# Performance work log

Hardware: AMD Instinct MI355X
Metric: run time of the kernel (lower is better)

Reference implementation:

```python
import jax, jax.numpy as jnp
import numpy as np

N_BINS = 50
FEATURE_ID = 0
EPS = 1e-7  # keras backend epsilon used by binary_crossentropy clipping


def setup_inputs() -> dict:
    key = jax.random.key(0)
    k1, k2 = jax.random.split(key)
    inputs = jax.random.normal(k1, (8_000_000, 4), dtype=jnp.float32)
    targets = jax.random.randint(k2, (8_000_000,), 0, 2, dtype=jnp.int32)
    return {"inputs": inputs, "targets": targets}


def _cut_forward(inputs, targets):
    # x: selected feature column, y: binary labels
    x = inputs[:, FEATURE_ID]
    y = targets
    N = x.shape[0]
    n_f = jnp.float32(N)

    x_min = jnp.min(x)
    x_max = jnp.max(x)
    E = N_BINS + 1
    edges = jnp.linspace(x_min, x_max, E)

    # Sort events once; prefix-sum of signal labels gives exact class counts
    # below/above any threshold (equivalent to the per-bin compare+count loop,
    # including the original's inclusive [lower, upper] double-counting of edges).
    order = jnp.argsort(x)
    xs = x[order]
    ys = (y[order] == 1).astype(jnp.float32)
    cs = jnp.concatenate([jnp.zeros((1,), jnp.float32), jnp.cumsum(ys)])  # [N+1]
    Ns = cs[-1]
    Nb = n_f - Ns

    r = jnp.searchsorted(xs, edges, side='right')  # count(x <= e)
    l = jnp.searchsorted(xs, edges, side='left')   # count(x <  e)
    ns_le = cs[r]
    ns_lt = cs[l]
    nb_le = r.astype(jnp.float32) - ns_le
    nb_lt = l.astype(jnp.float32) - ns_lt

    # hist[i] = count(lower[i] <= v <= upper[i]) per class
    hist0 = nb_le[1:] - nb_lt[:-1]  # background, [N_BINS]
    hist1 = ns_le[1:] - ns_lt[:-1]  # signal

    # candidate bin edges: sign-flip boundaries of hist0>hist1 with non-empty bins
    gt0 = hist0 > hist1
    cand0 = jnp.logical_xor(gt0[:-1], gt0[1:]) & (hist0[:-1] > 0)
    gt1 = hist1 > hist0
    cand1 = jnp.logical_xor(gt1[:-1], gt1[1:]) & (hist1[:-1] > 0)
    mask = jnp.zeros((E,), bool).at[1:N_BINS].set(cand0 | cand1)
    cnt = jnp.sum(mask)
    # original appends x_max when exactly one candidate survives
    mask = mask.at[-1].set(mask[-1] | (cnt == 1))

    # clipped BCE on hard 0/1 predictions reduces to a weighted error count:
    # correct sample -> -log(1-eps), wrong sample -> -log(eps)
    a = -jnp.log1p(jnp.float32(-EPS))
    b = -jnp.log(jnp.float32(EPS))

    def bce(correct):
        return ((n_f - correct) * b + correct * a) / n_f

    # per-edge losses for single-threshold cases
    c0 = ns_le + (Nb - nb_le)          # case 0: pred = (x <= c)
    c1 = (Ns - ns_lt) + nb_lt          # case 1: pred = (x >= c)
    # per-pair losses (i = lower cut, j = upper cut)
    c2 = (ns_le[None, :] - ns_lt[:, None]) + Nb - (nb_le[None, :] - nb_lt[:, None])
    c3 = ns_le[:, None] + (Ns - ns_lt[None, :]) + (nb_le[None, :] - nb_lt[:, None])

    L = jnp.stack([
        jnp.broadcast_to(bce(c0)[:, None], (E, E)),
        jnp.broadcast_to(bce(c1)[:, None], (E, E)),
        bce(c2),
        bce(c3),
    ])  # [4, E, E]
    per_pair_min = jnp.min(L, axis=0)
    per_pair_case = jnp.argmin(L, axis=0)

    idx = jnp.arange(E)
    valid = mask[:, None] & mask[None, :] & (idx[:, None] < idx[None, :])
    flat = jnp.argmin(jnp.where(valid, per_pair_min, jnp.inf))
    i = flat // E
    j = flat % E
    lower = edges[i]
    upper = edges[j]
    case = per_pair_case[i, j]

    pred0 = x <= lower
    pred1 = x >= lower
    pred2 = pred1 & (x <= upper)
    pred3 = pred0 | (x >= upper)
    y_pred = jnp.where(case == 0, pred0,
             jnp.where(case == 1, pred1,
             jnp.where(case == 2, pred2, pred3)))
    return y_pred


def reference(inputs, targets):
    return _cut_forward(inputs, targets).astype(jnp.int32)
```

## Files before the change

kernel.cpp:

```cpp
#include <hip/hip_runtime.h>
#include <math.h>
#include <stdint.h>

#define N_BINS 50
#define EDGE_N 51
#define HIST_N 52
#define NBLK 2048
#define NTHR 256

typedef unsigned int u32;
typedef unsigned short u16;
typedef unsigned char u8;
typedef float f32x4 __attribute__((ext_vector_type(4)));


#define KEEP16(v) asm volatile("" :: "v"(v))

__device__ __forceinline__ float edge_at(int e, float xmin, float xmax) {
  if (e >= N_BINS) return xmax;
  float step = __fdiv_rn((float)e, (float)N_BINS);
  float omst = __fsub_rn(1.0f, step);
  return __fadd_rn(__fmul_rn(xmin, omst), __fmul_rn(xmax, step));
}

__device__ __forceinline__ float bce_f(int c, float n_f, float aC, float bC) {
  float cf = (float)c;
  float t = __fadd_rn(__fmul_rn(__fsub_rn(n_f, cf), bC), __fmul_rn(cf, aC));
  return __fdiv_rn(t, n_f);
}

__device__ __forceinline__ void get_ab(float& aC, float& bC) {
  const double epsd = (double)1e-7f;
  aC = (float)(-log1p(-epsd));
  bC = (float)(-log(epsd));
}

__device__ __forceinline__ void global_minmax(const float* __restrict__ bmin,
                                              const float* __restrict__ bmax,
                                              float* s_red, float* s_mm) {
  const int tid = threadIdx.x;
  float m = INFINITY, M = -INFINITY;
  for (int i = tid; i < NBLK; i += NTHR) { m = fminf(m, bmin[i]); M = fmaxf(M, bmax[i]); }
  for (int off = 32; off; off >>= 1) {
    m = fminf(m, __shfl_down(m, off));
    M = fmaxf(M, __shfl_down(M, off));
  }
  int wid = tid >> 6;
  if ((tid & 63) == 0) { s_red[wid] = m; s_red[4 + wid] = M; }
  __syncthreads();
  if (tid == 0) {
    float mm = s_red[0], MM = s_red[4];
    for (int w = 1; w < NTHR / 64; ++w) { mm = fminf(mm, s_red[w]); MM = fmaxf(MM, s_red[4 + w]); }
    s_mm[0] = mm;
    s_mm[1] = MM;
  }
  __syncthreads();
}

template <int COMPACT>
__global__ void k_minmax(const f32x4* __restrict__ in4, int n,
                         float* __restrict__ bmin, float* __restrict__ bmax,
                         int* __restrict__ histU, int* __restrict__ histE,
                         float* __restrict__ xc) {
  const int tid = threadIdx.x, bid = blockIdx.x;
  const int gid = bid * NTHR + tid;
  const int T = NBLK * NTHR;
  if (bid == 0) {
    for (int i = tid; i < 2 * HIST_N; i += NTHR) histU[i] = 0;
    for (int i = tid; i < 2 * EDGE_N; i += NTHR) histE[i] = 0;
  }
  float vmin = INFINITY, vmax = -INFINITY;
#pragma unroll 4
  for (int i = gid; i < n; i += T) {
    f32x4 r = in4[i];
    KEEP16(r);
    float x = r.x;
    vmin = fminf(vmin, x);
    vmax = fmaxf(vmax, x);
    if (COMPACT) xc[i] = x;
  }
  for (int off = 32; off; off >>= 1) {
    vmin = fminf(vmin, __shfl_down(vmin, off));
    vmax = fmaxf(vmax, __shfl_down(vmax, off));
  }
  __shared__ float s_red[8];
  int wid = tid >> 6;
  if ((tid & 63) == 0) { s_red[wid] = vmin; s_red[4 + wid] = vmax; }
  __syncthreads();
  if (tid == 0) {
    float m = s_red[0], M = s_red[4];
    for (int w = 1; w < NTHR / 64; ++w) { m = fminf(m, s_red[w]); M = fmaxf(M, s_red[4 + w]); }
    bmin[bid] = m;
    bmax[bid] = M;
  }
}

template <int COMPACT>
__global__ void k_hist(const f32x4* __restrict__ in4, const float* __restrict__ xc,
                       const int* __restrict__ tgt, int n,
                       const float* __restrict__ bmin, const float* __restrict__ bmax,
                       int* __restrict__ histU, int* __restrict__ histE,
                       u8* __restrict__ codes) {
  __shared__ u16 ph[HIST_N][NTHR];
  __shared__ float s_edges[EDGE_N];
  __shared__ int shE[2 * EDGE_N];
  __shared__ float s_red[8];
  __shared__ float s_mm[2];
  const int tid = threadIdx.x, bid = blockIdx.x;
  global_minmax(bmin, bmax, s_red, s_mm);
  u32* ph32w = (u32*)&ph[0][0];
  for (int i = tid; i < HIST_N * (NTHR / 2); i += NTHR) ph32w[i] = 0;
  for (int i = tid; i < 2 * EDGE_N; i += NTHR) shE[i] = 0;
  const float xmin = s_mm[0], xmax = s_mm[1];
  if (tid < EDGE_N) s_edges[tid] = edge_at(tid, xmin, xmax);
  __syncthreads();
  const float delta = __fdiv_rn(__fsub_rn(xmax, xmin), (float)N_BINS);
  const float inv_delta = (delta > 0.0f) ? (1.0f / delta) : 0.0f;
  const int gid = bid * NTHR + tid;
  const int T = NBLK * NTHR;
  const int nv = n >> 2;
  const int base = nv << 2;
  const f32x4* __restrict__ xc4 = (const f32x4*)xc;
  const int4* __restrict__ tgt4 = (const int4*)tgt;
  uchar4* __restrict__ codes4 = (uchar4*)codes;
  for (int iv = gid; iv < nv; iv += T) {
    float xs[4];
    if (COMPACT) {
      f32x4 v = xc4[iv];
      xs[0] = v.x; xs[1] = v.y; xs[2] = v.z; xs[3] = v.w;
    } else {
      f32x4 a = in4[4 * iv + 0], b = in4[4 * iv + 1], c = in4[4 * iv + 2], d = in4[4 * iv + 3];
      xs[0] = a.x; xs[1] = b.x; xs[2] = c.x; xs[3] = d.x;
    }
    int4 tv = tgt4[iv];
    int ts[4] = {tv.x, tv.y, tv.z, tv.w};
    u8 cd[4];
#pragma unroll
    for (int k = 0; k < 4; ++k) {
      float x = xs[k];
      int cls = (ts[k] == 1) ? 0 : 1;
      int g = (int)((x - xmin) * inv_delta);
      g = max(0, min(g, EDGE_N));
      while (g < EDGE_N && s_edges[g] < x) ++g;
      while (g > 0 && s_edges[g - 1] >= x) --g;
      int eq = (g < EDGE_N && s_edges[g] == x) ? 1 : 0;
      ph[g][tid] = (u16)(ph[g][tid] + (1u << (cls * 8)));
      if (eq) atomicAdd(&shE[cls * EDGE_N + g], 1);
      cd[k] = (u8)(g | (eq << 6));
    }
    if (COMPACT) codes4[iv] = make_uchar4(cd[0], cd[1], cd[2], cd[3]);
  }
  if (bid == 0 && tid < (n - base)) {
    int i = base + tid;
    float x = COMPACT ? xc[i] : in4[i].x;
    int cls = (tgt[i] == 1) ? 0 : 1;
    int g = (int)((x - xmin) * inv_delta);
    g = max(0, min(g, EDGE_N));
    while (g < EDGE_N && s_edges[g] < x) ++g;
    while (g > 0 && s_edges[g - 1] >= x) --g;
    int eq = (g < EDGE_N && s_edges[g] == x) ? 1 : 0;
    ph[g][tid] = (u16)(ph[g][tid] + (1u << (cls * 8)));
    if (eq) atomicAdd(&shE[cls * EDGE_N + g], 1);
    if (COMPACT) codes[i] = (u8)(g | (eq << 6));
  }
  __syncthreads();
  if (tid < HIST_N) {
    const u32* ph32r = (const u32*)&ph[0][0];
    u32 c0 = 0, c1 = 0;
    for (int k2 = 0; k2 < NTHR / 2; ++k2) {
      int idx = (k2 + tid) & (NTHR / 2 - 1);
      u32 w = ph32r[tid * (NTHR / 2) + idx];
      c0 += (w & 0xFFu) + ((w >> 16) & 0xFFu);
      c1 += ((w >> 8) & 0xFFu) + ((w >> 24) & 0xFFu);
    }
    if (c0) atomicAdd(&histU[tid], (int)c0);
    if (c1) atomicAdd(&histU[HIST_N + tid], (int)c1);
  }
  for (int kk = tid; kk < 2 * EDGE_N; kk += NTHR) {
    int v = shE[kk];
    if (v) atomicAdd(&histE[kk], v);
  }
}

template <int COMPACT>
__global__ void k_decide_pred(const f32x4* __restrict__ in4, const u8* __restrict__ codes,
                              int n, const float* __restrict__ bmin,
                              const float* __restrict__ bmax,
                              const int* __restrict__ histU, const int* __restrict__ histE,
                              int* __restrict__ out) {
  __shared__ float s_red[8];
  __shared__ float s_mm[2];
  __shared__ int s_ns_le[EDGE_N], s_ns_lt[EDGE_N], s_nb_le[EDGE_N], s_nb_lt[EDGE_N];
  __shared__ int s_h0[N_BINS], s_h1[N_BINS];
  __shared__ unsigned char s_g0[N_BINS], s_g1[N_BINS];
  __shared__ unsigned char s_mask[EDGE_N];
  __shared__ float s_rv[NTHR];
  __shared__ int s_ri[NTHR];
  __shared__ int s_cut[3];
  const int tid = threadIdx.x, bid = blockIdx.x;

  global_minmax(bmin, bmax, s_red, s_mm);

  if (tid < 128) {
    const int lane = tid & 63;
    const int w = tid >> 6;
    int v = (lane < EDGE_N) ? histU[w * HIST_N + lane] : 0;
#pragma unroll
    for (int d = 1; d < 64; d <<= 1) {
      int t = __shfl_up(v, d);
      if (lane >= d) v += t;
    }
    if (lane < EDGE_N) {
      int e = histE[w * EDGE_N + lane];
      if (w == 0) { s_ns_le[lane] = v; s_ns_lt[lane] = v - e; }
      else        { s_nb_le[lane] = v; s_nb_lt[lane] = v - e; }
    }
  }
  if (tid < EDGE_N) s_mask[tid] = 0;
  __syncthreads();
  if (tid < N_BINS) {
    int h0 = s_nb_le[tid + 1] - s_nb_lt[tid];
    int h1 = s_ns_le[tid + 1] - s_ns_lt[tid];
    s_h0[tid] = h0;
    s_h1[tid] = h1;
    s_g0[tid] = h0 > h1;
    s_g1[tid] = h1 > h0;
  }
  __syncthreads();
  if (tid < 64) {
    bool cand = false;
    if (tid + 1 < N_BINS) {
      bool c0 = (s_g0[tid] != s_g0[tid + 1]) && (s_h0[tid] > 0);
      bool c1 = (s_g1[tid] != s_g1[tid + 1]) && (s_h1[tid] > 0);
      cand = c0 || c1;
      if (cand) s_mask[tid + 1] = 1;
    }
    unsigned long long bal = __ballot(cand);
    if (tid == 0 && __popcll(bal) == 1) s_mask[N_BINS] = 1;
  }
  __syncthreads();
  const int Ns = s_ns_le[EDGE_N - 1];
  const int Nb = n - Ns;
  float aC, bC;
  get_ab(aC, bC);
  const float n_f = (float)n;
  float best = INFINITY;
  int bestIdx = 0x7fffffff;
  for (int p = tid; p < EDGE_N * EDGE_N; p += NTHR) {
    int i = p / EDGE_N, j = p - i * EDGE_N;
    float v = INFINITY;
    if (s_mask[i] && s_mask[j] && i < j) {
      int c0 = s_ns_le[i] + (Nb - s_nb_le[i]);
      int c1 = Ns - s_ns_lt[i] + s_nb_lt[i];
      int c2 = s_ns_le[j] - s_ns_lt[i] + Nb - (s_nb_le[j] - s_nb_lt[i]);
      int c3 = s_ns_le[i] + Ns - s_ns_lt[j] + s_nb_le[j] - s_nb_lt[i];
      float L0 = bce_f(c0, n_f, aC, bC);
      float L1 = bce_f(c1, n_f, aC, bC);
      float L2 = bce_f(c2, n_f, aC, bC);
      float L3 = bce_f(c3, n_f, aC, bC);
      v = L0;
      if (L1 < v) v = L1;
      if (L2 < v) v = L2;
      if (L3 < v) v = L3;
    }
    if (v < best || (v == best && p < bestIdx)) { best = v; bestIdx = p; }
  }
  s_rv[tid] = best;
  s_ri[tid] = bestIdx;
  __syncthreads();
  for (int s = NTHR / 2; s > 0; s >>= 1) {
    if (tid < s) {
      float ov = s_rv[tid + s];
      int oi = s_ri[tid + s];
      if (ov < s_rv[tid] || (ov == s_rv[tid] && oi < s_ri[tid])) {
        s_rv[tid] = ov;
        s_ri[tid] = oi;
      }
    }
    __syncthreads();
  }
  if (tid == 0) {
    int p = s_ri[0];
    int i = p / EDGE_N, j = p - i * EDGE_N;
    int c0 = s_ns_le[i] + (Nb - s_nb_le[i]);
    int c1 = Ns - s_ns_lt[i] + s_nb_lt[i];
    int c2 = s_ns_le[j] - s_ns_lt[i] + Nb - (s_nb_le[j] - s_nb_lt[i]);
    int c3 = s_ns_le[i] + Ns - s_ns_lt[j] + s_nb_le[j] - s_nb_lt[i];
    float L0 = bce_f(c0, n_f, aC, bC);
    float L1 = bce_f(c1, n_f, aC, bC);
    float L2 = bce_f(c2, n_f, aC, bC);
    float L3 = bce_f(c3, n_f, aC, bC);
    int cs = 0;
    float m = L0;
    if (L1 < m) { m = L1; cs = 1; }
    if (L2 < m) { m = L2; cs = 2; }
    if (L3 < m) { m = L3; cs = 3; }
    s_cut[0] = cs;
    s_cut[1] = i;
    s_cut[2] = j;
  }
  __syncthreads();

  const int cs = s_cut[0], ci = s_cut[1], cj = s_cut[2];
  const int gid = bid * NTHR + tid;
  const int T = NBLK * NTHR;
  if (COMPACT) {
    const uchar4* __restrict__ c4 = (const uchar4*)codes;
    int4* __restrict__ out4 = (int4*)out;
    const int nv = n >> 2;
    for (int iv = gid; iv < nv; iv += T) {
      uchar4 c = c4[iv];
      u8 bys[4] = {c.x, c.y, c.z, c.w};
      int r[4];
#pragma unroll
      for (int b = 0; b < 4; ++b) {
        int u = (int)(bys[b] & 63u);
        int v = u + (int)(bys[b] >> 6);
        bool p0 = (u <= ci), p1 = (ci < v);
        bool p = (cs == 0) ? p0 : (cs == 1) ? p1 : (cs == 2) ? (p1 && (u <= cj)) : (p0 || (cj < v));
        r[b] = p ? 1 : 0;
      }
      out4[iv] = make_int4(r[0], r[1], r[2], r[3]);
    }
    const int cbase = (n >> 2) << 2;
    if (bid == 0 && tid < (n - cbase)) {
      int i = cbase + tid;
      u32 by = codes[i];
      int u = (int)(by & 63u);
      int v = u + (int)(by >> 6);
      bool p0 = (u <= ci), p1 = (ci < v);
      bool p = (cs == 0) ? p0 : (cs == 1) ? p1 : (cs == 2) ? (p1 && (u <= cj)) : (p0 || (cj < v));
      out[i] = p ? 1 : 0;
    }
  } else {
    const float xmin = s_mm[0], xmax = s_mm[1];
    const float lower = edge_at(ci, xmin, xmax);
    const float upper = edge_at(cj, xmin, xmax);
    for (int i = gid; i < n; i += T) {
      f32x4 r = in4[i];
      float x = r.x;
      bool p;
      if (cs == 0) p = (x <= lower);
      else if (cs == 1) p = (x >= lower);
      else if (cs == 2) p = (x >= lower) && (x <= upper);
      else p = (x <= lower) || (x >= upper);
      out[i] = p ? 1 : 0;
    }
  }
}

extern "C" void kernel_launch(void* const* d_in, const int* in_sizes, int n_in,
                              void* d_out, int out_size, void* d_ws, size_t ws_size,
                              hipStream_t stream) {
  const f32x4* in4 = (const f32x4*)d_in[0];
  const int* tgt = (const int*)d_in[1];
  int n = in_sizes[1];
  int* out = (int*)d_out;
  char* ws = (char*)d_ws;
  float* bmin = (float*)ws;
  float* bmax = (float*)(ws + 8192);
  int* histU = (int*)(ws + 16448);
  int* histE = histU + 2 * HIST_N;
  u8* codes = (u8*)(ws + 32768);
  size_t xcOff = ((size_t)32768 + (size_t)n + 15) & ~(size_t)15;
  float* xc = (float*)(ws + xcOff);
  const bool compact = ws_size >= xcOff + (size_t)n * 4u;

  if (compact) {
    k_minmax<1><<<NBLK, NTHR, 0, stream>>>(in4, n, bmin, bmax, histU, histE, xc);
    k_hist<1><<<NBLK, NTHR, 0, stream>>>(in4, xc, tgt, n, bmin, bmax, histU, histE, codes);
    k_decide_pred<1><<<NBLK, NTHR, 0, stream>>>(in4, codes, n, bmin, bmax, histU, histE, out);
  } else {
    k_minmax<0><<<NBLK, NTHR, 0, stream>>>(in4, n, bmin, bmax, histU, histE, nullptr);
    k_hist<0><<<NBLK, NTHR, 0, stream>>>(in4, nullptr, tgt, n, bmin, bmax, histU, histE, nullptr);
    k_decide_pred<0><<<NBLK, NTHR, 0, stream>>>(in4, nullptr, n, bmin, bmax, histU, histE, out);
  }
}
```

Baseline: 108.6 us.

## Fuse three kernels into one cooperative persistent kernel with grid barriers

Merges the min/max, histogram and decide/predict kernels into a single cooperative launch. Inter-phase dependencies are handled by custom grid barriers built on atomic counters. Global min/max now goes through order-preserving encoded atomicMin/Max instead of a per-block array, and histogram atomics are spread over 16 replicas to reduce contention. A small init kernel is added and the grid is capped by an occupancy query, which trades launch gaps and extra global round trips for spin-wait barrier cost and fewer blocks.

```diff
diff --git a/kernel.cpp b/kernel.cpp
--- a/kernel.cpp
+++ b/kernel.cpp
@@ -5,8 +5,9 @@
 #define N_BINS 50
 #define EDGE_N 51
 #define HIST_N 52
-#define NBLK 2048
 #define NTHR 256
+#define MAXBLK 1280
+#define NREP 16
 
 typedef unsigned int u32;
 typedef unsigned short u16;
@@ -15,6 +16,15 @@
 
 
 #define KEEP16(v) asm volatile("" :: "v"(v))
+
+__device__ __forceinline__ u32 f32_enc(float f) {
+  u32 u = __float_as_uint(f);
+  return (u & 0x80000000u) ? ~u : (u | 0x80000000u);
+}
+__device__ __forceinline__ float f32_dec(u32 k) {
+  u32 u = (k & 0x80000000u) ? (k & 0x7fffffffu) : ~k;
+  return __uint_as_float(u);
+}
 
 __device__ __forceinline__ float edge_at(int e, float xmin, float xmax) {
   if (e >= N_BINS) return xmax;
@@ -35,40 +45,58 @@
   bC = (float)(-log(epsd));
 }
 
-__device__ __forceinline__ void global_minmax(const float* __restrict__ bmin,
-                                              const float* __restrict__ bmax,
-                                              float* s_red, float* s_mm) {
-  const int tid = threadIdx.x;
-  float m = INFINITY, M = -INFINITY;
-  for (int i = tid; i < NBLK; i += NTHR) { m = fminf(m, bmin[i]); M = fmaxf(M, bmax[i]); }
-  for (int off = 32; off; off >>= 1) {
-    m = fminf(m, __shfl_down(m, off));
-    M = fmaxf(M, __shfl_down(M, off));
-  }
-  int wid = tid >> 6;
-  if ((tid & 63) == 0) { s_red[wid] = m; s_red[4 + wid] = M; }
-  __syncthreads();
-  if (tid == 0) {
-    float mm = s_red[0], MM = s_red[4];
-    for (int w = 1; w < NTHR / 64; ++w) { mm = fminf(mm, s_red[w]); MM = fmaxf(MM, s_red[4 + w]); }
-    s_mm[0] = mm;
-    s_mm[1] = MM;
-  }
-  __syncthreads();
+__device__ __forceinline__ void gbar(int* cnt, int nblk, int bid) {
+  __syncthreads();
+  if (threadIdx.x == 0) {
+    __threadfence();
+    __hip_atomic_fetch_add(&cnt[bid & (NREP - 1)], 1, __ATOMIC_RELAXED,
+                           __HIP_MEMORY_SCOPE_AGENT);
+    int s;
+    do {
+      s = 0;
+#pragma unroll
+      for (int k = 0; k < NREP; ++k)
+        s += __hip_atomic_load(&cnt[k], __ATOMIC_RELAXED, __HIP_MEMORY_SCOPE_AGENT);
+      if (s < nblk) __builtin_amdgcn_s_sleep(4);
+    } while (s < nblk);
+    __threadfence();
+  }
+  __syncthreads();
+}
+
+__global__ void k_init(u32* __restrict__ wsu, int* __restrict__ histU,
+                       int* __restrict__ histE) {
+  int t = threadIdx.x;
+  if (t == 0) { wsu[0] = 0xFFFFFFFFu; wsu[1] = 0u; }
+  if (t < 32) ((int*)(wsu + 2))[t] = 0;
+  for (int i = t; i < NREP * 2 * HIST_N; i += NTHR) histU[i] = 0;
+  for (int i = t; i < NREP * 2 * EDGE_N; i += NTHR) histE[i] = 0;
 }
 
 template <int COMPACT>
-__global__ void k_minmax(const f32x4* __restrict__ in4, int n,
-                         float* __restrict__ bmin, float* __restrict__ bmax,
-                         int* __restrict__ histU, int* __restrict__ histE,
-                         float* __restrict__ xc) {
+__global__ void __launch_bounds__(NTHR, 5)
+k_all(const f32x4* __restrict__ in4, const int* __restrict__ tgt, int n, int nblk,
+      u32* __restrict__ wsu, int* __restrict__ histU, int* __restrict__ histE,
+      u8* __restrict__ codes, float* __restrict__ xc, int* __restrict__ out) {
+  __shared__ u16 ph[HIST_N][NTHR];
+  __shared__ float s_edges[EDGE_N];
+  __shared__ int shE[2 * EDGE_N];
+  __shared__ float s_red[8];
+  __shared__ float s_mm[2];
+  __shared__ int s_ns_le[EDGE_N], s_ns_lt[EDGE_N], s_nb_le[EDGE_N], s_nb_lt[EDGE_N];
+  __shared__ int s_h0[N_BINS], s_h1[N_BINS];
+  __shared__ unsigned char s_g0[N_BINS], s_g1[N_BINS];
+  __shared__ unsigned char s_mask[EDGE_N];
+  __shared__ float s_rv[NTHR];
+  __shared__ int s_ri[NTHR];
+  __shared__ int s_cut[3];
+
   const int tid = threadIdx.x, bid = blockIdx.x;
   const int gid = bid * NTHR + tid;
-  const int T = NBLK * NTHR;
-  if (bid == 0) {
-    for (int i = tid; i < 2 * HIST_N; i += NTHR) histU[i] = 0;
-    for (int i = tid; i < 2 * EDGE_N; i += NTHR) histE[i] = 0;
-  }
+  const int T = nblk * NTHR;
+  int* cnt1 = (int*)(wsu + 2);
+  int* cnt2 = (int*)(wsu + 18);
+
   float vmin = INFINITY, vmax = -INFINITY;
 #pragma unroll 4
   for (int i = gid; i < n; i += T) {
@@ -79,66 +107,75 @@
     vmax = fmaxf(vmax, x);
     if (COMPACT) xc[i] = x;
   }
+  {
+    u32* p32 = (u32*)&ph[0][0];
+    for (int i = tid; i < HIST_N * (NTHR / 2); i += NTHR) p32[i] = 0;
+    for (int i = tid; i < 2 * EDGE_N; i += NTHR) shE[i] = 0;
+  }
   for (int off = 32; off; off >>= 1) {
     vmin = fminf(vmin, __shfl_down(vmin, off));
     vmax = fmaxf(vmax, __shfl_down(vmax, off));
   }
-  __shared__ float s_red[8];
-  int wid = tid >> 6;
-  if ((tid & 63) == 0) { s_red[wid] = vmin; s_red[4 + wid] = vmax; }
+  {
+    int wid = tid >> 6;
+    if ((tid & 63) == 0) { s_red[wid] = vmin; s_red[4 + wid] = vmax; }
+  }
   __syncthreads();
   if (tid == 0) {
     float m = s_red[0], M = s_red[4];
     for (int w = 1; w < NTHR / 64; ++w) { m = fminf(m, s_red[w]); M = fmaxf(M, s_red[4 + w]); }
-    bmin[bid] = m;
-    bmax[bid] = M;
-  }
-}
-
-template <int COMPACT>
-__global__ void k_hist(const f32x4* __restrict__ in4, const float* __restrict__ xc,
-                       const int* __restrict__ tgt, int n,
-                       const float* __restrict__ bmin, const float* __restrict__ bmax,
-                       int* __restrict__ histU, int* __restrict__ histE,
-                       u8* __restrict__ codes) {
-  __shared__ u16 ph[HIST_N][NTHR];
-  __shared__ float s_edges[EDGE_N];
-  __shared__ int shE[2 * EDGE_N];
-  __shared__ float s_red[8];
-  __shared__ float s_mm[2];
-  const int tid = threadIdx.x, bid = blockIdx.x;
-  global_minmax(bmin, bmax, s_red, s_mm);
-  u32* ph32w = (u32*)&ph[0][0];
-  for (int i = tid; i < HIST_N * (NTHR / 2); i += NTHR) ph32w[i] = 0;
-  for (int i = tid; i < 2 * EDGE_N; i += NTHR) shE[i] = 0;
+    atomicMin(&wsu[0], f32_enc(m));
+    atomicMax(&wsu[1], f32_enc(M));
+  }
+  gbar(cnt1, nblk, bid);
+  if (tid == 0) {
+    s_mm[0] = f32_dec(__hip_atomic_load(&wsu[0], __ATOMIC_RELAXED, __HIP_MEMORY_SCOPE_AGENT));
+    s_mm[1] = f32_dec(__hip_atomic_load(&wsu[1], __ATOMIC_RELAXED, __HIP_MEMORY_SCOPE_AGENT));
+  }
+  __syncthreads();
+
   const float xmin = s_mm[0], xmax = s_mm[1];
   if (tid < EDGE_N) s_edges[tid] = edge_at(tid, xmin, xmax);
   __syncthreads();
-  const float delta = __fdiv_rn(__fsub_rn(xmax, xmin), (float)N_BINS);
-  const float inv_delta = (delta > 0.0f) ? (1.0f / delta) : 0.0f;
-  const int gid = bid * NTHR + tid;
-  const int T = NBLK * NTHR;
-  const int nv = n >> 2;
-  const int base = nv << 2;
-  const f32x4* __restrict__ xc4 = (const f32x4*)xc;
-  const int4* __restrict__ tgt4 = (const int4*)tgt;
-  uchar4* __restrict__ codes4 = (uchar4*)codes;
-  for (int iv = gid; iv < nv; iv += T) {
-    float xs[4];
-    if (COMPACT) {
-      f32x4 v = xc4[iv];
-      xs[0] = v.x; xs[1] = v.y; xs[2] = v.z; xs[3] = v.w;
-    } else {
-      f32x4 a = in4[4 * iv + 0], b = in4[4 * iv + 1], c = in4[4 * iv + 2], d = in4[4 * iv + 3];
-      xs[0] = a.x; xs[1] = b.x; xs[2] = c.x; xs[3] = d.x;
-    }
-    int4 tv = tgt4[iv];
-    int ts[4] = {tv.x, tv.y, tv.z, tv.w};
-    u8 cd[4];
+  {
+    const float delta = __fdiv_rn(__fsub_rn(xmax, xmin), (float)N_BINS);
+    const float inv_delta = (delta > 0.0f) ? (1.0f / delta) : 0.0f;
+    const int nv = n >> 2;
+    const int base = nv << 2;
+    const f32x4* __restrict__ xc4 = (const f32x4*)xc;
+    const int4* __restrict__ tgt4 = (const int4*)tgt;
+    uchar4* __restrict__ codes4 = (uchar4*)codes;
+    for (int iv = gid; iv < nv; iv += T) {
+      float xs[4];
+      if (COMPACT) {
+        f32x4 v = xc4[iv];
+        xs[0] = v.x; xs[1] = v.y; xs[2] = v.z; xs[3] = v.w;
+      } else {
+        f32x4 a = in4[4 * iv + 0], b = in4[4 * iv + 1], c = in4[4 * iv + 2], d = in4[4 * iv + 3];
+        xs[0] = a.x; xs[1] = b.x; xs[2] = c.x; xs[3] = d.x;
+      }
+      int4 tv = tgt4[iv];
+      int ts[4] = {tv.x, tv.y, tv.z, tv.w};
+      u8 cd[4];
 #pragma unroll
-    for (int k = 0; k < 4; ++k) {
-      float x = xs[k];
-      int cls = (ts[k] == 1) ? 0 : 1;
+      for (int k = 0; k < 4; ++k) {
+        float x = xs[k];
+        int cls = (ts[k] == 1) ? 0 : 1;
+        int g = (int)((x - xmin) * inv_delta);
+        g = max(0, min(g, EDGE_N));
+        while (g < EDGE_N && s_edges[g] < x) ++g;
+        while (g > 0 && s_edges[g - 1] >= x) --g;
+        int eq = (g < EDGE_N && s_edges[g] == x) ? 1 : 0;
+        ph[g][tid] = (u16)(ph[g][tid] + (1u << (cls * 8)));
+        if (eq) atomicAdd(&shE[cls * EDGE_N + g], 1);
+        cd[k] = (u8)(g | (eq << 6));
+      }
+      if (COMPACT) codes4[iv] = make_uchar4(cd[0], cd[1], cd[2], cd[3]);
+    }
+    if (bid == 0 && tid < (n - base)) {
+      int i = base + tid;
+      float x = COMPACT ? xc[i] : in4[i].x;
+      int cls = (tgt[i] == 1) ? 0 : 1;
       int g = (int)((x - xmin) * inv_delta);
       g = max(0, min(g, EDGE_N));
       while (g < EDGE_N && s_edges[g] < x) ++g;
@@ -146,72 +183,45 @@
       int eq = (g < EDGE_N && s_edges[g] == x) ? 1 : 0;
       ph[g][tid] = (u16)(ph[g][tid] + (1u << (cls * 8)));
       if (eq) atomicAdd(&shE[cls * EDGE_N + g], 1);
-      cd[k] = (u8)(g | (eq << 6));
-    }
-    if (COMPACT) codes4[iv] = make_uchar4(cd[0], cd[1], cd[2], cd[3]);
-  }
-  if (bid == 0 && tid < (n - base)) {
-    int i = base + tid;
-    float x = COMPACT ? xc[i] : in4[i].x;
-    int cls = (tgt[i] == 1) ? 0 : 1;
-    int g = (int)((x - xmin) * inv_delta);
-    g = max(0, min(g, EDGE_N));
-    while (g < EDGE_N && s_edges[g] < x) ++g;
-    while (g > 0 && s_edges[g - 1] >= x) --g;
-    int eq = (g < EDGE_N && s_edges[g] == x) ? 1 : 0;
-    ph[g][tid] = (u16)(ph[g][tid] + (1u << (cls * 8)));
-    if (eq) atomicAdd(&shE[cls * EDGE_N + g], 1);
-    if (COMPACT) codes[i] = (u8)(g | (eq << 6));
-  }
-  __syncthreads();
-  if (tid < HIST_N) {
-    const u32* ph32r = (const u32*)&ph[0][0];
-    u32 c0 = 0, c1 = 0;
-    for (int k2 = 0; k2 < NTHR / 2; ++k2) {
-      int idx = (k2 + tid) & (NTHR / 2 - 1);
-      u32 w = ph32r[tid * (NTHR / 2) + idx];
-      c0 += (w & 0xFFu) + ((w >> 16) & 0xFFu);
-      c1 += ((w >> 8) & 0xFFu) + ((w >> 24) & 0xFFu);
-    }
-    if (c0) atomicAdd(&histU[tid], (int)c0);
-    if (c1) atomicAdd(&histU[HIST_N + tid], (int)c1);
-  }
-  for (int kk = tid; kk < 2 * EDGE_N; kk += NTHR) {
-    int v = shE[kk];
-    if (v) atomicAdd(&histE[kk], v);
-  }
-}
-
-template <int COMPACT>
-__global__ void k_decide_pred(const f32x4* __restrict__ in4, const u8* __restrict__ codes,
-                              int n, const float* __restrict__ bmin,
-                              const float* __restrict__ bmax,
-                              const int* __restrict__ histU, const int* __restrict__ histE,
-                              int* __restrict__ out) {
-  __shared__ float s_red[8];
-  __shared__ float s_mm[2];
-  __shared__ int s_ns_le[EDGE_N], s_ns_lt[EDGE_N], s_nb_le[EDGE_N], s_nb_lt[EDGE_N];
-  __shared__ int s_h0[N_BINS], s_h1[N_BINS];
-  __shared__ unsigned char s_g0[N_BINS], s_g1[N_BINS];
-  __shared__ unsigned char s_mask[EDGE_N];
-  __shared__ float s_rv[NTHR];
-  __shared__ int s_ri[NTHR];
-  __shared__ int s_cut[3];
-  const int tid = threadIdx.x, bid = blockIdx.x;
-
-  global_minmax(bmin, bmax, s_red, s_mm);
+      if (COMPACT) codes[i] = (u8)(g | (eq << 6));
+    }
+    __syncthreads();
+    int* hU = histU + (bid & (NREP - 1)) * (2 * HIST_N);
+    int* hE = histE + (bid & (NREP - 1)) * (2 * EDGE_N);
+    if (tid < HIST_N) {
+      const u32* p32 = (const u32*)&ph[0][0];
+      u32 c0 = 0, c1 = 0;
+      for (int k2 = 0; k2 < NTHR / 2; ++k2) {
+        int idx = (k2 + tid) & (NTHR / 2 - 1);
+        u32 w = p32[tid * (NTHR / 2) + idx];
+        c0 += (w & 0xFFu) + ((w >> 16) & 0xFFu);
+        c1 += ((w >> 8) & 0xFFu) + ((w >> 24) & 0xFFu);
+      }
+      if (c0) atomicAdd(&hU[tid], (int)c0);
+      if (c1) atomicAdd(&hU[HIST_N + tid], (int)c1);
+    }
+    for (int kk = tid; kk < 2 * EDGE_N; kk += NTHR) {
+      int v = shE[kk];
+      if (v) atomicAdd(&hE[kk], v);
+    }
+  }
+  gbar(cnt2, nblk, bid);
 
   if (tid < 128) {
     const int lane = tid & 63;
     const int w = tid >> 6;
-    int v = (lane < EDGE_N) ? histU[w * HIST_N + lane] : 0;
+    int v = 0;
+    if (lane < EDGE_N) {
+      for (int r = 0; r < NREP; ++r) v += histU[r * (2 * HIST_N) + w * HIST_N + lane];
+    }
 #pragma unroll
     for (int d = 1; d < 64; d <<= 1) {
       int t = __shfl_up(v, d);
       if (lane >= d) v += t;
     }
     if (lane < EDGE_N) {
-      int e = histE[w * EDGE_N + lane];
+      int e = 0;
+      for (int r = 0; r < NREP; ++r) e += histE[r * (2 * EDGE_N) + w * EDGE_N + lane];
       if (w == 0) { s_ns_le[lane] = v; s_ns_lt[lane] = v - e; }
       else        { s_nb_le[lane] = v; s_nb_lt[lane] = v - e; }
     }
@@ -302,8 +312,6 @@
   __syncthreads();
 
   const int cs = s_cut[0], ci = s_cut[1], cj = s_cut[2];
-  const int gid = bid * NTHR + tid;
-  const int T = NBLK * NTHR;
   if (COMPACT) {
     const uchar4* __restrict__ c4 = (const uchar4*)codes;
     int4* __restrict__ out4 = (int4*)out;
@@ -333,7 +341,6 @@
       out[i] = p ? 1 : 0;
     }
   } else {
-    const float xmin = s_mm[0], xmax = s_mm[1];
     const float lower = edge_at(ci, xmin, xmax);
     const float upper = edge_at(cj, xmin, xmax);
     for (int i = gid; i < n; i += T) {
@@ -357,22 +364,33 @@
   int n = in_sizes[1];
   int* out = (int*)d_out;
   char* ws = (char*)d_ws;
-  float* bmin = (float*)ws;
-  float* bmax = (float*)(ws + 8192);
-  int* histU = (int*)(ws + 16448);
-  int* histE = histU + 2 * HIST_N;
-  u8* codes = (u8*)(ws + 32768);
-  size_t xcOff = ((size_t)32768 + (size_t)n + 15) & ~(size_t)15;
+  u32* wsu = (u32*)ws;
+  int* histU = (int*)(ws + 256);
+  int* histE = (int*)(ws + 256 + NREP * 2 * HIST_N * 4);
+  u8* codes = (u8*)(ws + 16384);
+  size_t xcOff = ((size_t)16384 + (size_t)n + 15) & ~(size_t)15;
   float* xc = (float*)(ws + xcOff);
   const bool compact = ws_size >= xcOff + (size_t)n * 4u;
 
+  int maxb = 0;
+  hipError_t oe = hipOccupancyMaxActiveBlocksPerMultiprocessor(
+      &maxb, compact ? (const void*)k_all<1> : (const void*)k_all<0>, NTHR, 0);
+  int nblk = MAXBLK;
+  if (oe == hipSuccess && maxb > 0) {
+    int cap = maxb * 256;
+    if (cap < nblk) nblk = cap;
+  } else {
+    nblk = 1024;
+  }
+
+  k_init<<<1, NTHR, 0, stream>>>(wsu, histU, histE);
   if (compact) {
-    k_minmax<1><<<NBLK, NTHR, 0, stream>>>(in4, n, bmin, bmax, histU, histE, xc);
-    k_hist<1><<<NBLK, NTHR, 0, stream>>>(in4, xc, tgt, n, bmin, bmax, histU, histE, codes);
-    k_decide_pred<1><<<NBLK, NTHR, 0, stream>>>(in4, codes, n, bmin, bmax, histU, histE, out);
+    void* args[10] = {(void*)&in4, (void*)&tgt, (void*)&n, (void*)&nblk, (void*)&wsu,
+                      (void*)&histU, (void*)&histE, (void*)&codes, (void*)&xc, (void*)&out};
+    hipLaunchCooperativeKernel((void*)k_all<1>, dim3(nblk), dim3(NTHR), args, 0, stream);
   } else {
-    k_minmax<0><<<NBLK, NTHR, 0, stream>>>(in4, n, bmin, bmax, histU, histE, nullptr);
-    k_hist<0><<<NBLK, NTHR, 0, stream>>>(in4, nullptr, tgt, n, bmin, bmax, histU, histE, nullptr);
-    k_decide_pred<0><<<NBLK, NTHR, 0, stream>>>(in4, nullptr, n, bmin, bmax, histU, histE, out);
-  }
-}
+    void* args[10] = {(void*)&in4, (void*)&tgt, (void*)&n, (void*)&nblk, (void*)&wsu,
+                      (void*)&histU, (void*)&histE, (void*)&codes, (void*)&xc, (void*)&out};
+    hipLaunchCooperativeKernel((void*)k_all<0>, dim3(nblk), dim3(NTHR), args, 0, stream);
+  }
+}
```

New measurement: 414.1 us. 281% more time.
